# Performance work log

Hardware: AMD Instinct MI355X
Metric: run time of the kernel (lower is better)

The kernel has to match this reference:

```python
import jax, jax.numpy as jnp
import numpy as np

BLOCK = 64      # block_size
NRAND = 3       # num_random_blocks
NUM_HEAD = 16
HEAD_DIM = 64
HIDDEN = 1024
PEN = -10000.0  # HF attn_mask_penalty


def _sparse_attn(q, k, v, band_mask, from_mask, to_mask, blocked_mask, rand_attn):
    # q,k,v: [B,H,S,D]; BigBird block-sparse attention (HF math).
    B, H, S, D = q.shape
    b, r = BLOCK, NRAND
    n = S // b
    rsd = 1.0 / (D ** 0.5)

    bq = q.reshape(B, H, n, b, D)
    bk = k.reshape(B, H, n, b, D)
    bv = v.reshape(B, H, n, b, D)

    bi = jnp.arange(B)[:, None, None, None]
    hi = jnp.arange(H)[None, :, None, None]
    # gathered random key/value blocks: [B,H,n-2,r*b,D]
    gk = bk[bi, hi, rand_attn].reshape(B, H, n - 2, r * b, D)
    gv = bv[bi, hi, rand_attn].reshape(B, H, n - 2, r * b, D)
    # random-block mask: [B,H,n-2,b,r*b]
    rm = blocked_mask[bi, rand_attn].reshape(B, H, n - 2, r * b)
    rand_mask = jnp.einsum("blq,bhlk->bhlqk", blocked_mask[:, 1:-1], rm)

    ones = lambda shp: jnp.ones(shp, q.dtype)

    # ---- first query block: attends to everything ----
    p = jnp.einsum("bhqd,bhkd->bhqk", bq[:, :, 0], k) * rsd + (1.0 - to_mask) * PEN
    c0 = jnp.einsum("bhqk,bhkd->bhqd", jax.nn.softmax(p, -1), v)[:, :, None]

    # ---- second query block: blocks 0,1,2,last + random ----
    k1 = jnp.concatenate([bk[:, :, 0], bk[:, :, 1], bk[:, :, 2], bk[:, :, -1], gk[:, :, 0]], axis=2)
    v1 = jnp.concatenate([bv[:, :, 0], bv[:, :, 1], bv[:, :, 2], bv[:, :, -1], gv[:, :, 0]], axis=2)
    p = jnp.einsum("bhqd,bhkd->bhqk", bq[:, :, 1], k1) * rsd
    seq_pad = jnp.concatenate([to_mask[..., :3 * b], to_mask[..., -b:], ones((B, 1, 1, r * b))], axis=3)
    rand_pad = jnp.concatenate([ones((B, H, b, 4 * b)), rand_mask[:, :, 0]], axis=3)
    p = p + (1.0 - jnp.minimum(seq_pad, rand_pad)) * PEN
    c1 = jnp.einsum("bhqk,bhkd->bhqd", jax.nn.softmax(p, -1), v1)[:, :, None]

    # ---- middle blocks 2..n-3: band(3 blocks) + first + last + random ----
    ek = jnp.concatenate([bk[:, :, 1:-3], bk[:, :, 2:-2], bk[:, :, 3:-1]], axis=3)  # [B,H,n-4,3b,D]
    ev = jnp.concatenate([bv[:, :, 1:-3], bv[:, :, 2:-2], bv[:, :, 3:-1]], axis=3)
    mq = bq[:, :, 2:-2]                                                              # [B,H,n-4,b,D]
    inner = jnp.einsum("bhlqd,bhlkd->bhlqk", mq, ek) * rsd + (1.0 - band_mask) * PEN
    randp = jnp.einsum("bhlqd,bhlkd->bhlqk", mq, gk[:, :, 1:-1]) * rsd + (1.0 - rand_mask[:, :, 1:-1]) * PEN
    firstp = jnp.einsum("bhlqd,bhkd->bhlqk", mq, bk[:, :, 0]) * rsd + (1.0 - to_mask[..., :b][:, :, None]) * PEN
    lastp = jnp.einsum("bhlqd,bhkd->bhlqk", mq, bk[:, :, -1]) * rsd + (1.0 - to_mask[..., -b:][:, :, None]) * PEN
    band = jnp.concatenate([firstp, inner, randp, lastp], axis=-1)  # [B,H,n-4,b,(5+r)*b]
    a = jax.nn.softmax(band, -1)
    cm = jnp.einsum("bhlqk,bhlkd->bhlqd", a[..., b:4 * b], ev)
    cm = cm + jnp.einsum("bhlqk,bhlkd->bhlqd", a[..., 4 * b:-b], gv[:, :, 1:-1])
    cm = cm + jnp.einsum("bhlqk,bhkd->bhlqd", a[..., :b], bv[:, :, 0])
    cm = cm + jnp.einsum("bhlqk,bhkd->bhlqd", a[..., -b:], bv[:, :, -1])

    # ---- second-last query block: blocks 0,-3,-2,-1 + random ----
    k2 = jnp.concatenate([bk[:, :, 0], bk[:, :, -3], bk[:, :, -2], bk[:, :, -1], gk[:, :, -1]], axis=2)
    v2 = jnp.concatenate([bv[:, :, 0], bv[:, :, -3], bv[:, :, -2], bv[:, :, -1], gv[:, :, -1]], axis=2)
    p = jnp.einsum("bhqd,bhkd->bhqk", bq[:, :, -2], k2) * rsd
    seq_pad = jnp.concatenate([to_mask[..., :b], to_mask[..., -3 * b:], ones((B, 1, 1, r * b))], axis=3)
    rand_pad = jnp.concatenate([ones((B, H, b, 4 * b)), rand_mask[:, :, -1]], axis=3)
    p = p + (1.0 - jnp.minimum(seq_pad, rand_pad)) * PEN
    c2 = jnp.einsum("bhqk,bhkd->bhqd", jax.nn.softmax(p, -1), v2)[:, :, None]

    # ---- last query block: attends to everything ----
    p = jnp.einsum("bhqd,bhkd->bhqk", bq[:, :, -1], k) * rsd + (1.0 - to_mask) * PEN
    c3 = jnp.einsum("bhqk,bhkd->bhqd", jax.nn.softmax(p, -1), v)[:, :, None]

    ctx = jnp.concatenate([c0, c1, cm, c2, c3], axis=2).reshape(B, H, S, D)
    ctx = ctx * from_mask  # [B,1,S,1]
    return ctx.transpose(0, 2, 1, 3).reshape(B, S, H * D)


def setup_inputs() -> dict:
    key = jax.random.key(0)
    ks = jax.random.split(key, 12)
    B, L = 2, 4064
    S = 4096
    n = S // BLOCK
    sc = 0.02
    inp = {
        "X": jax.random.normal(ks[0], (B, L, HIDDEN), jnp.float32),
        "Wq": jax.random.normal(ks[1], (HIDDEN, NUM_HEAD * HEAD_DIM), jnp.float32) * sc,
        "b_q": jnp.zeros((NUM_HEAD * HEAD_DIM,), jnp.float32),
        "Wk": jax.random.normal(ks[2], (HIDDEN, NUM_HEAD * HEAD_DIM), jnp.float32) * sc,
        "b_k": jnp.zeros((NUM_HEAD * HEAD_DIM,), jnp.float32),
        "Wv": jax.random.normal(ks[3], (HIDDEN, NUM_HEAD * HEAD_DIM), jnp.float32) * sc,
        "b_v": jnp.zeros((NUM_HEAD * HEAD_DIM,), jnp.float32),
        "Wo": jax.random.normal(ks[4], (NUM_HEAD * HEAD_DIM, HIDDEN), jnp.float32) * sc,
        "b_o": jnp.zeros((HIDDEN,), jnp.float32),
        "band_mask": jnp.ones((B, 1, n - 4, BLOCK, 3 * BLOCK), jnp.float32),
        "from_mask": jnp.ones((B, 1, S, 1), jnp.float32),
        "to_mask": jnp.ones((B, 1, 1, S), jnp.float32),
        "blocked_encoder_mask": jnp.ones((B, n, BLOCK), jnp.float32),
        "rand_attn": jax.random.randint(ks[5], (B, NUM_HEAD, n - 2, NRAND), 0, n, jnp.int32),
    }
    return inp


def reference(X, Wq, b_q, Wk, b_k, Wv, b_v, Wo, b_o,
              band_mask, from_mask, to_mask, blocked_encoder_mask, rand_attn):
    B, L, _ = X.shape
    pad = BLOCK - L % BLOCK  # matches torch wrapper (pads full block if L % b == 0)
    Xp = jnp.pad(X, ((0, 0), (0, pad), (0, 0)))
    S = L + pad

    def proj(W, bias):
        return (Xp @ W + bias).reshape(B, S, NUM_HEAD, HEAD_DIM).transpose(0, 2, 1, 3)

    q, k, v = proj(Wq, b_q), proj(Wk, b_k), proj(Wv, b_v)
    attn = _sparse_attn(q, k, v, band_mask, from_mask, to_mask, blocked_encoder_mask, rand_attn)
    out = attn @ Wo + b_o
    return out[:, :L]
```

## Files before the change

### kernel.cpp

```cpp
#include <hip/hip_runtime.h>

#define BB 2
#define SEQ 4096
#define LQ 4064
#define HID 1024
#define NH 16
#define HD 64
#define NB 64
#define BLK 64
#define NR 3
#define PENV -10000.0f

typedef __bf16 bf16;
typedef __bf16 bf16x8 __attribute__((ext_vector_type(8)));
typedef float floatx4 __attribute__((ext_vector_type(4)));

#define MEMFENCE asm volatile("" ::: "memory")

__device__ inline floatx4 mfma16(bf16x8 a, bf16x8 b, floatx4 c) {
    return __builtin_amdgcn_mfma_f32_16x16x32_bf16(a, b, c, 0, 0, 0);
}

__device__ inline void async_ld16(const bf16* g, bf16* l) {
    __builtin_amdgcn_global_load_lds(
        (const __attribute__((address_space(1))) unsigned int*)g,
        (__attribute__((address_space(3))) unsigned int*)l, 16, 0, 0);
}

__device__ inline void stage_k2(const bf16* kkbh, bf16* dst, int kb0, int kb1, int tid) {
    #pragma unroll
    for (int it = 0; it < 2; it++) {
        int o = (it * 256 + tid) * 16;
        int row = o >> 7;
        int c16 = (o >> 4) & 7;
        int srcel = row * 64 + ((c16 ^ (row & 7)) << 3);
        async_ld16(kkbh + (size_t)kb0 * (BLK * HD) + srcel, dst + (o >> 1));
        async_ld16(kkbh + (size_t)kb1 * (BLK * HD) + srcel, dst + 4096 + (o >> 1));
    }
}

__global__ __launch_bounds__(256) void cast_pad_x(const float* __restrict__ X,
                                                  bf16* __restrict__ Xp) {
    int t = blockIdx.x * 256 + threadIdx.x;
    int c4 = t & 255;
    int row = t >> 8;
    int b = row >> 12;
    int s = row & 4095;
    float4 v = make_float4(0.f, 0.f, 0.f, 0.f);
    if (s < LQ) {
        v = reinterpret_cast<const float4*>(X + ((size_t)(b * LQ + s)) * HID)[c4];
    }
    union { bf16 h[4]; uint2 u; } o;
    o.h[0] = (bf16)v.x; o.h[1] = (bf16)v.y; o.h[2] = (bf16)v.z; o.h[3] = (bf16)v.w;
    *reinterpret_cast<uint2*>(Xp + (size_t)row * HID + c4 * 4) = o.u;
}

__global__ __launch_bounds__(256) void transpose_w(const float* __restrict__ Wq,
                                                   const float* __restrict__ Wk,
                                                   const float* __restrict__ Wv,
                                                   const float* __restrict__ Wo,
                                                   bf16* __restrict__ WqkvT,
                                                   bf16* __restrict__ WoT) {
    __shared__ float tile[64][65];
    int sel = blockIdx.z;
    const float* src = (sel == 0) ? Wq : (sel == 1) ? Wk : (sel == 2) ? Wv : Wo;
    bf16* dst = (sel < 3) ? (WqkvT + (size_t)sel * HID * HID) : WoT;
    int j0 = blockIdx.x * 64, k0 = blockIdx.y * 64;
    int tx = threadIdx.x, ty = threadIdx.y;
    for (int i = 0; i < 16; i++) {
        int k = ty + i * 4;
        tile[k][tx] = src[(size_t)(k0 + k) * HID + j0 + tx];
    }
    __syncthreads();
    for (int i = 0; i < 16; i++) {
        int j = ty + i * 4;
        dst[(size_t)(j0 + j) * HID + k0 + tx] = (bf16)tile[tx][j];
    }
}

__global__ __launch_bounds__(256) void transpose_band(const float* __restrict__ band,
                                                      float* __restrict__ bandT) {
    __shared__ float tile[64][65];
    int kt = blockIdx.x;
    int lrow = blockIdx.y;
    int b = blockIdx.z;
    const float* src = band + ((size_t)(b * (NB - 4) + lrow) * BLK) * 192;
    float* dst = bandT + ((size_t)(b * (NB - 4) + lrow) * 192) * BLK;
    int tx = threadIdx.x, ty = threadIdx.y;
    for (int i = 0; i < 16; i++) {
        int qq = i * 4 + ty;
        tile[qq][tx] = src[(size_t)qq * 192 + kt * 64 + tx];
    }
    __syncthreads();
    for (int i = 0; i < 16; i++) {
        int k = i * 4 + ty;
        dst[(size_t)(kt * 64 + k) * BLK + tx] = tile[tx][k];
    }
}

__global__ __launch_bounds__(256) void mask_viol(const float* __restrict__ tom,
                                                 const float* __restrict__ blocked,
                                                 const float* __restrict__ band,
                                                 int* __restrict__ flags) {
    int which = blockIdx.y, b = blockIdx.z;
    const float* src;
    size_t n;
    if (which == 0)      { src = tom     + (size_t)b * SEQ;                  n = SEQ; }
    else if (which == 1) { src = blocked + (size_t)b * NB * BLK;             n = NB * BLK; }
    else                 { src = band    + (size_t)b * (NB - 4) * BLK * 192; n = (size_t)(NB - 4) * BLK * 192; }
    const float4* s4 = (const float4*)src;
    size_t n4 = n >> 2;
    int bad = 0;
    for (size_t i = blockIdx.x * 256 + threadIdx.x; i < n4; i += 240 * 256) {
        float4 v = s4[i];
        bad |= (v.x != 1.0f) | (v.y != 1.0f) | (v.z != 1.0f) | (v.w != 1.0f);
    }
    if (__any(bad) && (threadIdx.x & 63) == 0)
        atomicOr(&flags[which * BB + b], 1);
}

__global__ __launch_bounds__(256) void gemm_qkv(const bf16* __restrict__ Xp,
                                                const bf16* __restrict__ WT,
                                                const float* __restrict__ bq,
                                                const float* __restrict__ bk,
                                                const float* __restrict__ bv,
                                                bf16* __restrict__ qo,
                                                bf16* __restrict__ ko,
                                                bf16* __restrict__ vt) {
    __shared__ __align__(16) char smem[36864];
    bf16* As = (bf16*)smem;
    bf16* Bs = As + 128 * 64;
    int tid = threadIdx.x;
    int wave = tid >> 6, lane = tid & 63;
    int quad = lane >> 4, lm = lane & 15;
    int id = blockIdx.x;
    int xcd = id & 7, slot = id >> 3;
    int tile_m = (xcd * 8 + (slot & 7)) * 128;
    int tile_n = (slot >> 3) * 128;
    int wm = (wave & 1) * 64, wn = (wave >> 1) * 64;

    floatx4 acc[4][4] = {};

    for (int k0 = 0; k0 < HID; k0 += 64) {
        __syncthreads();
        for (int it = 0; it < 4; it++) {
            int c = it * 256 + tid;
            int row = c >> 3, col = (c & 7) * 8;
            async_ld16(Xp + (size_t)(tile_m + row) * HID + k0 + col, &As[c * 8]);
            async_ld16(WT + (size_t)(tile_n + row) * HID + k0 + col, &Bs[c * 8]);
        }
        __syncthreads();
        for (int ks = 0; ks < 64; ks += 32) {
            bf16x8 a[4], b[4];
            for (int i = 0; i < 4; i++)
                a[i] = *reinterpret_cast<const bf16x8*>(&As[(wm + i * 16 + lm) * 64 + ks + quad * 8]);
            for (int j = 0; j < 4; j++)
                b[j] = *reinterpret_cast<const bf16x8*>(&Bs[(wn + j * 16 + lm) * 64 + ks + quad * 8]);
            for (int i = 0; i < 4; i++)
                for (int j = 0; j < 4; j++)
                    acc[i][j] = mfma16(a[i], b[j], acc[i][j]);
        }
    }

    int which = tile_n >> 10;
    int hc_base = (tile_n + wn) & 1023;
    int h = hc_base >> 6;
    const float* bias = (which == 0) ? bq : (which == 1) ? bk : bv;
    __syncthreads();
    bf16* ep = (bf16*)smem + wave * (64 * 72);

    if (which < 2) {
        #pragma unroll
        for (int i = 0; i < 4; i++)
            #pragma unroll
            for (int j = 0; j < 4; j++) {
                float bsv = bias[hc_base + j * 16 + lm];
                #pragma unroll
                for (int r = 0; r < 4; r++) {
                    float val = acc[i][j][r] + bsv;
                    if (which == 0) val *= 0.125f;
                    ep[(i * 16 + quad * 4 + r) * 72 + j * 16 + lm] = (bf16)val;
                }
            }
        __builtin_amdgcn_wave_barrier();
        int s_glob = tile_m + wm + lane;
        int b_ = s_glob >> 12, s = s_glob & 4095;
        bf16* dstb = ((which == 0) ? qo : ko) + ((size_t)((b_ * NH + h) * SEQ + s)) * HD;
        #pragma unroll
        for (int c = 0; c < 8; c++)
            *reinterpret_cast<uint4*>(dstb + c * 8) =
                *reinterpret_cast<const uint4*>(ep + lane * 72 + c * 8);
    } else {
        #pragma unroll
        for (int i = 0; i < 4; i++)
            #pragma unroll
            for (int j = 0; j < 4; j++) {
                float bsv = bias[hc_base + j * 16 + lm];
                #pragma unroll
                for (int r = 0; r < 4; r++) {
                    float val = acc[i][j][r] + bsv;
                    ep[(j * 16 + lm) * 72 + i * 16 + quad * 4 + r] = (bf16)val;
                }
            }
        __builtin_amdgcn_wave_barrier();
        int s_base = tile_m + wm;
        int b_ = s_base >> 12, s0 = s_base & 4095;
        bf16* dstb = vt + ((size_t)((b_ * NH + h) * HD + lane)) * SEQ + s0;
        #pragma unroll
        for (int c = 0; c < 8; c++)
            *reinterpret_cast<uint4*>(dstb + c * 8) =
                *reinterpret_cast<const uint4*>(ep + lane * 72 + c * 8);
    }
}

__global__ __launch_bounds__(256, 2) void attn_kernel(const bf16* __restrict__ q,
                                                      const bf16* __restrict__ kk,
                                                      const bf16* __restrict__ vt,
                                                      const float* __restrict__ bandT,
                                                      const float* __restrict__ fromm,
                                                      const float* __restrict__ tom,
                                                      const float* __restrict__ blocked,
                                                      const int* __restrict__ rand_attn,
                                                      const int* __restrict__ flags,
                                                      bf16* __restrict__ attn) {
    __shared__ __align__(16) char smem[32768];
    bf16* sK = (bf16*)smem;

    int tid = threadIdx.x, wave = tid >> 6, lane = tid & 63;
    int quad = lane >> 4, lm = lane & 15;
    int sw = lm & 7;
    int bh = blockIdx.x;
    int b = bh >> 4, h = bh & 15;
    size_t bh_base = (size_t)bh * SEQ * HD;
    int x = blockIdx.y;
    bool fullmode = (x < 8);
    int l, sub;
    if (fullmode) { l = (x >> 2) ? (NB - 1) : 0; sub = x & 3; }
    else          { l = x - 7;                   sub = wave;  }

    bool do_to = flags[b] != 0;
    bool do_bl = flags[BB + b] != 0;
    bool do_bd = flags[2 * BB + b] != 0;

    unsigned long long kbp = 0ull;
    unsigned int typ_p = 0u;
    if (!fullmode) {
        int base;
        if (l == 1) {
            kbp = (1ull << 8) | (2ull << 16) | ((unsigned long long)(NB - 1) << 24);
            base = 4;
        } else if (l == NB - 2) {
            kbp = ((unsigned long long)(NB - 3) << 8) | ((unsigned long long)(NB - 2) << 16) |
                  ((unsigned long long)(NB - 1) << 24);
            base = 4;
        } else {
            kbp = ((unsigned long long)(l - 1) << 8) | ((unsigned long long)l << 16) |
                  ((unsigned long long)(l + 1) << 24) | ((unsigned long long)(NB - 1) << 32);
            typ_p = (1u << 4) | (2u << 8) | (3u << 12);
            base = 5;
        }
        const int* ra = rand_attn + ((size_t)(b * NH + h) * (NB - 2) + (l - 1)) * NR;
        #pragma unroll
        for (int r = 0; r < NR; r++) {
            int rv = __builtin_amdgcn_readfirstlane(ra[r]);
            kbp   |= (unsigned long long)(rv & 63) << ((base + r) * 8);
            typ_p |= 4u << ((base + r) * 4);
        }
        for (int i = base + NR; i < 8; i++) typ_p |= 5u << (i * 4);
    }

    bf16x8 aq0 = *reinterpret_cast<const bf16x8*>(
        q + bh_base + (size_t)(l * BLK + sub * 16 + lm) * HD + quad * 8);
    bf16x8 aq1 = *reinterpret_cast<const bf16x8*>(
        q + bh_base + (size_t)(l * BLK + sub * 16 + lm) * HD + 32 + quad * 8);
    float mq = blocked[((size_t)b * NB + l) * BLK + sub * 16 + lm];

    if (!fullmode) {
        MEMFENCE;
        int a0 = (int)((kbp >> 0) & 63),  a1 = (int)((kbp >> 8) & 63);
        int b0 = (int)((kbp >> 16) & 63), b1 = (int)((kbp >> 24) & 63);
        stage_k2(kk + bh_base, sK + 0,    a0, a1, tid);
        stage_k2(kk + bh_base, sK + 8192, b0, b1, tid);
        MEMFENCE;
    }

    floatx4 ctx[4] = {};
    float mrun = -1e30f, lrun = 0.f;

    int sbase = ((quad & 1) << 5) + lm;
    int fhi = quad >> 1;

    int nch = fullmode ? 8 : 4;
    for (int ch = 0; ch < nch; ch++) {
        int i0 = ch * 2, i1 = i0 + 1;
        int kb0, kb1, ty0, ty1;
        if (fullmode) {
            kb0 = __builtin_amdgcn_readfirstlane(wave * 16 + i0);
            kb1 = kb0 + 1;
            ty0 = 0; ty1 = 0;
        } else {
            kb0 = __builtin_amdgcn_readfirstlane((int)((kbp >> (i0 * 8)) & 63));
            kb1 = __builtin_amdgcn_readfirstlane((int)((kbp >> (i1 * 8)) & 63));
            ty0 = (int)((typ_p >> (i0 * 4)) & 15);
            ty1 = (int)((typ_p >> (i1 * 4)) & 15);
        }

        const bf16* v0p = vt + bh_base + (size_t)kb0 * BLK;
        bf16x8 vf0[4][2];
        #pragma unroll
        for (int dj = 0; dj < 4; dj++) {
            vf0[dj][0] = *reinterpret_cast<const bf16x8*>(v0p + (size_t)(dj * 16 + lm) * SEQ + quad * 8);
            vf0[dj][1] = *reinterpret_cast<const bf16x8*>(v0p + (size_t)(dj * 16 + lm) * SEQ + 32 + quad * 8);
        }
        MEMFENCE;

        floatx4 sc[2][4];
        if (!fullmode) {
            if (ch < 3) asm volatile("s_waitcnt vmcnt(8)" ::: "memory");
            else        asm volatile("s_waitcnt vmcnt(16)" ::: "memory");
            __builtin_amdgcn_s_barrier();
            const bf16* kbuf = sK + (ch & 1) * 8192;
            #pragma unroll
            for (int u = 0; u < 2; u++) {
                bf16x8 ka[4], kb_[4];
                #pragma unroll
                for (int f = 0; f < 4; f++) {
                    int rowb = (f * 16 + lm) * 64;
                    ka[f]  = *reinterpret_cast<const bf16x8*>(
                        kbuf + u * 4096 + rowb + ((quad ^ sw) << 3));
                    kb_[f] = *reinterpret_cast<const bf16x8*>(
                        kbuf + u * 4096 + rowb + (((quad | 4) ^ sw) << 3));
                }
                #pragma unroll
                for (int f = 0; f < 4; f++) {
                    floatx4 z = {0.f, 0.f, 0.f, 0.f};
                    z = mfma16(ka[f], aq0, z);
                    z = mfma16(kb_[f], aq1, z);
                    sc[u][f] = z;
                }
            }
        } else {
            const bf16* k0p = kk + bh_base + (size_t)kb0 * (BLK * HD);
            const bf16* k1p = kk + bh_base + (size_t)kb1 * (BLK * HD);
            bf16x8 kfa[2][4], kfb[2][4];
            #pragma unroll
            for (int f = 0; f < 4; f++) {
                kfa[0][f] = *reinterpret_cast<const bf16x8*>(k0p + (f * 16 + lm) * HD + quad * 8);
                kfb[0][f] = *reinterpret_cast<const bf16x8*>(k0p + (f * 16 + lm) * HD + 32 + quad * 8);
                kfa[1][f] = *reinterpret_cast<const bf16x8*>(k1p + (f * 16 + lm) * HD + quad * 8);
                kfb[1][f] = *reinterpret_cast<const bf16x8*>(k1p + (f * 16 + lm) * HD + 32 + quad * 8);
            }
            #pragma unroll
            for (int u = 0; u < 2; u++)
                #pragma unroll
                for (int f = 0; f < 4; f++) {
                    floatx4 z = {0.f, 0.f, 0.f, 0.f};
                    z = mfma16(kfa[u][f], aq0, z);
                    z = mfma16(kfb[u][f], aq1, z);
                    sc[u][f] = z;
                }
        }

        const bf16* v1p = vt + bh_base + (size_t)kb1 * BLK;
        bf16x8 vf1[4][2];
        #pragma unroll
        for (int dj = 0; dj < 4; dj++) {
            vf1[dj][0] = *reinterpret_cast<const bf16x8*>(v1p + (size_t)(dj * 16 + lm) * SEQ + quad * 8);
            vf1[dj][1] = *reinterpret_cast<const bf16x8*>(v1p + (size_t)(dj * 16 + lm) * SEQ + 32 + quad * 8);
        }
        MEMFENCE;

        {
            int kbs[2] = {kb0, kb1};
            int tys[2] = {ty0, ty1};
            #pragma unroll
            for (int u = 0; u < 2; u++) {
                int kb = kbs[u], typ = tys[u];
                if (typ == 0) {
                    if (do_to) {
                        #pragma unroll
                        for (int f = 0; f < 4; f++) {
                            float4 t4 = *reinterpret_cast<const float4*>(
                                tom + (size_t)b * SEQ + kb * BLK + f * 16 + quad * 4);
                            sc[u][f][0] += (1.f - t4.x) * PENV;
                            sc[u][f][1] += (1.f - t4.y) * PENV;
                            sc[u][f][2] += (1.f - t4.z) * PENV;
                            sc[u][f][3] += (1.f - t4.w) * PENV;
                        }
                    }
                } else if (typ == 4) {
                    if (do_bl) {
                        #pragma unroll
                        for (int f = 0; f < 4; f++) {
                            float4 t4 = *reinterpret_cast<const float4*>(
                                blocked + ((size_t)b * NB + kb) * BLK + f * 16 + quad * 4);
                            sc[u][f][0] += (1.f - mq * t4.x) * PENV;
                            sc[u][f][1] += (1.f - mq * t4.y) * PENV;
                            sc[u][f][2] += (1.f - mq * t4.z) * PENV;
                            sc[u][f][3] += (1.f - mq * t4.w) * PENV;
                        }
                    }
                } else if (typ != 5) {
                    if (do_bd) {
                        int t = typ - 1;
                        const float* bp = bandT + ((size_t)(b * (NB - 4) + (l - 2)) * 192 + t * 64) * BLK;
                        #pragma unroll
                        for (int f = 0; f < 4; f++)
                            #pragma unroll
                            for (int r = 0; r < 4; r++) {
                                float bm = bp[(size_t)(f * 16 + quad * 4 + r) * BLK + sub * 16 + lm];
                                sc[u][f][r] += (1.f - bm) * PENV;
                            }
                    }
                } else {
                    #pragma unroll
                    for (int f = 0; f < 4; f++)
                        #pragma unroll
                        for (int r = 0; r < 4; r++) sc[u][f][r] += PENV;
                }
            }
        }

        float mx = -1e30f;
        #pragma unroll
        for (int u = 0; u < 2; u++)
            #pragma unroll
            for (int f = 0; f < 4; f++)
                #pragma unroll
                for (int r = 0; r < 4; r++) mx = fmaxf(mx, sc[u][f][r]);
        float a16 = __shfl_xor(mx, 16, 64);
        float a32 = __shfl_xor(mx, 32, 64);
        float a48 = __shfl_xor(mx, 48, 64);
        mx = fmaxf(fmaxf(mx, a16), fmaxf(a32, a48));
        float mnew = fmaxf(mrun, mx);
        float scale = __expf(mrun - mnew);
        #pragma unroll
        for (int dj = 0; dj < 4; dj++) ctx[dj] *= scale;
        mrun = mnew;

        float rs = 0.f;
        uint2 pk[2][4];
        #pragma unroll
        for (int u = 0; u < 2; u++)
            #pragma unroll
            for (int f = 0; f < 4; f++) {
                float p0 = __expf(sc[u][f][0] - mnew);
                float p1 = __expf(sc[u][f][1] - mnew);
                float p2 = __expf(sc[u][f][2] - mnew);
                float p3 = __expf(sc[u][f][3] - mnew);
                rs += (p0 + p1) + (p2 + p3);
                union { bf16 hh[4]; uint2 u2; } pu;
                pu.hh[0] = (bf16)p0; pu.hh[1] = (bf16)p1;
                pu.hh[2] = (bf16)p2; pu.hh[3] = (bf16)p3;
                pk[u][f] = pu.u2;
            }
        lrun = lrun * scale + rs;

        bf16x8 pb[2][2];
        #pragma unroll
        for (int u = 0; u < 2; u++) {
            unsigned g0x[4], g0y[4], g1x[4], g1y[4];
            #pragma unroll
            for (int f = 0; f < 4; f++) {
                g0x[f] = (unsigned)__shfl((int)pk[u][f].x, sbase, 64);
                g0y[f] = (unsigned)__shfl((int)pk[u][f].y, sbase, 64);
                g1x[f] = (unsigned)__shfl((int)pk[u][f].x, sbase + 16, 64);
                g1y[f] = (unsigned)__shfl((int)pk[u][f].y, sbase + 16, 64);
            }
            union { unsigned v[4]; bf16x8 hv; } lo, hi;
            lo.v[0] = fhi ? g0x[1] : g0x[0];
            lo.v[1] = fhi ? g0y[1] : g0y[0];
            lo.v[2] = fhi ? g1x[1] : g1x[0];
            lo.v[3] = fhi ? g1y[1] : g1y[0];
            hi.v[0] = fhi ? g0x[3] : g0x[2];
            hi.v[1] = fhi ? g0y[3] : g0y[2];
            hi.v[2] = fhi ? g1x[3] : g1x[2];
            hi.v[3] = fhi ? g1y[3] : g1y[2];
            pb[u][0] = lo.hv;
            pb[u][1] = hi.hv;
        }

        if (!fullmode && ch >= 1 && ch + 1 < 4) {
            int na = __builtin_amdgcn_readfirstlane((int)((kbp >> ((ch + 1) * 16)) & 63));
            int nb = __builtin_amdgcn_readfirstlane((int)((kbp >> ((ch + 1) * 16 + 8)) & 63));
            stage_k2(kk + bh_base, sK + ((ch + 1) & 1) * 8192, na, nb, tid);
            MEMFENCE;
        }

        #pragma unroll
        for (int dj = 0; dj < 4; dj++) {
            ctx[dj] = mfma16(vf0[dj][0], pb[0][0], ctx[dj]);
            ctx[dj] = mfma16(vf0[dj][1], pb[0][1], ctx[dj]);
        }
        #pragma unroll
        for (int dj = 0; dj < 4; dj++) {
            ctx[dj] = mfma16(vf1[dj][0], pb[1][0], ctx[dj]);
            ctx[dj] = mfma16(vf1[dj][1], pb[1][1], ctx[dj]);
        }
    }

    {
        float b16 = __shfl_xor(lrun, 16, 64);
        float b32 = __shfl_xor(lrun, 32, 64);
        float b48 = __shfl_xor(lrun, 48, 64);
        lrun = (lrun + b16) + (b32 + b48);
    }

    if (!fullmode) {
        int sq = l * BLK + sub * 16 + lm;
        float w = (1.f / lrun) * fromm[(size_t)b * SEQ + sq];
        bf16* dst = attn + ((size_t)(b * SEQ + sq)) * HID + h * HD;
        #pragma unroll
        for (int dj = 0; dj < 4; dj++) {
            union { bf16 hh[4]; uint2 u2; } o;
            #pragma unroll
            for (int r = 0; r < 4; r++) o.hh[r] = (bf16)(ctx[dj][r] * w);
            *reinterpret_cast<uint2*>(dst + dj * 16 + quad * 4) = o.u2;
        }
    } else {
        float* ctxL = (float*)smem;
        float* mL   = (float*)(smem + 16384);
        float* lL   = (float*)(smem + 16640);
        __syncthreads();
        #pragma unroll
        for (int dj = 0; dj < 4; dj++)
            #pragma unroll
            for (int r = 0; r < 4; r++)
                ctxL[wave * 1024 + (dj * 16 + quad * 4 + r) * 16 + lm] = ctx[dj][r];
        if (quad == 0) { mL[wave * 16 + lm] = mrun; lL[wave * 16 + lm] = lrun; }
        __syncthreads();
        int qq = tid & 15, dbase = (tid >> 4) * 4;
        float M = -1e30f;
        for (int w = 0; w < 4; w++) M = fmaxf(M, mL[w * 16 + qq]);
        float e[4], Lt = 0.f;
        for (int w = 0; w < 4; w++) { e[w] = __expf(mL[w * 16 + qq] - M); Lt += lL[w * 16 + qq] * e[w]; }
        int sq = l * BLK + sub * 16 + qq;
        float wgt = (1.f / Lt) * fromm[(size_t)b * SEQ + sq];
        union { bf16 hh[4]; uint2 u2; } o;
        #pragma unroll
        for (int dd = 0; dd < 4; dd++) {
            float acc = 0.f;
            for (int w = 0; w < 4; w++) acc += ctxL[w * 1024 + (dbase + dd) * 16 + qq] * e[w];
            o.hh[dd] = (bf16)(acc * wgt);
        }
        *reinterpret_cast<uint2*>(attn + ((size_t)(b * SEQ + sq)) * HID + h * HD + dbase) = o.u2;
    }
}

__global__ __launch_bounds__(256) void gemm_out(const bf16* __restrict__ A,
                                                const bf16* __restrict__ WoT,
                                                const float* __restrict__ bo,
                                                float* __restrict__ out) {
    __shared__ __align__(16) bf16 As[128 * 64];
    __shared__ __align__(16) bf16 Bs[128 * 64];
    int tid = threadIdx.x;
    int wave = tid >> 6, lane = tid & 63;
    int quad = lane >> 4, lm = lane & 15;
    int id = blockIdx.x;
    int xcd = id & 7, slot = id >> 3;
    int tile_m = (xcd * 8 + (slot & 7)) * 128;
    int tile_n = (slot >> 3) * 128;
    int wm = (wave & 1) * 64, wn = (wave >> 1) * 64;

    floatx4 acc[4][4] = {};

    for (int k0 = 0; k0 < HID; k0 += 64) {
        __syncthreads();
        for (int it = 0; it < 4; it++) {
            int c = it * 256 + tid;
            int row = c >> 3, col = (c & 7) * 8;
            async_ld16(A + (size_t)(tile_m + row) * HID + k0 + col, &As[c * 8]);
            async_ld16(WoT + (size_t)(tile_n + row) * HID + k0 + col, &Bs[c * 8]);
        }
        __syncthreads();
        for (int ks = 0; ks < 64; ks += 32) {
            bf16x8 a[4], b[4];
            for (int i = 0; i < 4; i++)
                a[i] = *reinterpret_cast<const bf16x8*>(&As[(wm + i * 16 + lm) * 64 + ks + quad * 8]);
            for (int j = 0; j < 4; j++)
                b[j] = *reinterpret_cast<const bf16x8*>(&Bs[(wn + j * 16 + lm) * 64 + ks + quad * 8]);
            for (int i = 0; i < 4; i++)
                for (int j = 0; j < 4; j++)
                    acc[i][j] = mfma16(a[i], b[j], acc[i][j]);
        }
    }

    for (int i = 0; i < 4; i++) {
        for (int j = 0; j < 4; j++) {
            int nn = tile_n + wn + j * 16 + lm;
            float bsv = bo[nn];
            for (int r = 0; r < 4; r++) {
                int mm = tile_m + wm + i * 16 + quad * 4 + r;
                int b_ = mm >> 12, s = mm & 4095;
                if (s < LQ)
                    out[((size_t)(b_ * LQ + s)) * HID + nn] = acc[i][j][r] + bsv;
            }
        }
    }
}

extern "C" void kernel_launch(void* const* d_in, const int* in_sizes, int n_in,
                              void* d_out, int out_size, void* d_ws, size_t ws_size,
                              hipStream_t stream) {
    const float* X       = (const float*)d_in[0];
    const float* Wq      = (const float*)d_in[1];
    const float* bq      = (const float*)d_in[2];
    const float* Wk      = (const float*)d_in[3];
    const float* bk      = (const float*)d_in[4];
    const float* Wv      = (const float*)d_in[5];
    const float* bv      = (const float*)d_in[6];
    const float* Wo      = (const float*)d_in[7];
    const float* bo      = (const float*)d_in[8];
    const float* band    = (const float*)d_in[9];
    const float* fromm   = (const float*)d_in[10];
    const float* tom     = (const float*)d_in[11];
    const float* blocked = (const float*)d_in[12];
    const int*   randa   = (const int*)d_in[13];
    float* out = (float*)d_out;

    char* ws = (char*)d_ws;
    bf16* Xp    = (bf16*)(ws + 0);
    bf16* WqkvT = (bf16*)(ws + 16777216);
    bf16* WoT   = (bf16*)(ws + 23068672);
    bf16* qb    = (bf16*)(ws + 25165824);
    bf16* kb    = (bf16*)(ws + 41943040);
    bf16* vtb   = (bf16*)(ws + 58720256);
    bf16* attnb = Xp;
    float* bandT = (float*)WqkvT;
    int* flagsp = (int*)(ws + 16777216 + 5898240);

    cast_pad_x<<<dim3(8192), dim3(256), 0, stream>>>(X, Xp);
    transpose_w<<<dim3(16, 16, 4), dim3(64, 4), 0, stream>>>(Wq, Wk, Wv, Wo, WqkvT, WoT);
    gemm_qkv<<<dim3(1536), dim3(256), 0, stream>>>(Xp, WqkvT, bq, bk, bv, qb, kb, vtb);
    transpose_band<<<dim3(3, NB - 4, BB), dim3(64, 4), 0, stream>>>(band, bandT);
    hipMemsetAsync(flagsp, 0, 3 * BB * sizeof(int), stream);
    mask_viol<<<dim3(240, 3, BB), dim3(256), 0, stream>>>(tom, blocked, band, flagsp);
    attn_kernel<<<dim3(BB * NH, 70), dim3(256), 0, stream>>>(qb, kb, vtb, bandT, fromm, tom,
                                                             blocked, randa, flagsp, attnb);
    gemm_out<<<dim3(512), dim3(256), 0, stream>>>(attnb, WoT, bo, out);
}
```

Before: 341.7 us.

## Double-buffer output GEMM LDS tiles and raise wave priority around MFMA blocks

The output projection GEMM now uses two LDS buffers, so the async global-to-LDS load for the next K tile is issued while MFMAs run on the current one. This removes one barrier per iteration and hides load latency. In the attention kernel, s_setprio brackets the QK and PV MFMA sections so waves doing matrix work get scheduling priority. The GEMM doubles its LDS use to 64KB, which may lower occupancy. The next tile's loads are issued without an explicit wait before the tile is consumed, so correctness depends on the barrier draining outstanding loads.

```diff
diff --git a/kernel.cpp b/kernel.cpp
--- a/kernel.cpp
+++ b/kernel.cpp
@@ -320,6 +320,7 @@
             else        asm volatile("s_waitcnt vmcnt(16)" ::: "memory");
             __builtin_amdgcn_s_barrier();
             const bf16* kbuf = sK + (ch & 1) * 8192;
+            __builtin_amdgcn_s_setprio(1);
             #pragma unroll
             for (int u = 0; u < 2; u++) {
                 bf16x8 ka[4], kb_[4];
@@ -339,6 +340,7 @@
                     sc[u][f] = z;
                 }
             }
+            __builtin_amdgcn_s_setprio(0);
         } else {
             const bf16* k0p = kk + bh_base + (size_t)kb0 * (BLK * HD);
             const bf16* k1p = kk + bh_base + (size_t)kb1 * (BLK * HD);
@@ -350,6 +352,7 @@
                 kfa[1][f] = *reinterpret_cast<const bf16x8*>(k1p + (f * 16 + lm) * HD + quad * 8);
                 kfb[1][f] = *reinterpret_cast<const bf16x8*>(k1p + (f * 16 + lm) * HD + 32 + quad * 8);
             }
+            __builtin_amdgcn_s_setprio(1);
             #pragma unroll
             for (int u = 0; u < 2; u++)
                 #pragma unroll
@@ -359,6 +362,7 @@
                     z = mfma16(kfb[u][f], aq1, z);
                     sc[u][f] = z;
                 }
+            __builtin_amdgcn_s_setprio(0);
         }
 
         const bf16* v1p = vt + bh_base + (size_t)kb1 * BLK;
@@ -487,6 +491,7 @@
             MEMFENCE;
         }
 
+        __builtin_amdgcn_s_setprio(1);
         #pragma unroll
         for (int dj = 0; dj < 4; dj++) {
             ctx[dj] = mfma16(vf0[dj][0], pb[0][0], ctx[dj]);
@@ -497,6 +502,7 @@
             ctx[dj] = mfma16(vf1[dj][0], pb[1][0], ctx[dj]);
             ctx[dj] = mfma16(vf1[dj][1], pb[1][1], ctx[dj]);
         }
+        __builtin_amdgcn_s_setprio(0);
     }
 
     {
@@ -551,8 +557,7 @@
                                                 const bf16* __restrict__ WoT,
                                                 const float* __restrict__ bo,
                                                 float* __restrict__ out) {
-    __shared__ __align__(16) bf16 As[128 * 64];
-    __shared__ __align__(16) bf16 Bs[128 * 64];
+    __shared__ __align__(16) char smem[65536];
     int tid = threadIdx.x;
     int wave = tid >> 6, lane = tid & 63;
     int quad = lane >> 4, lm = lane & 15;
@@ -564,15 +569,33 @@
 
     floatx4 acc[4][4] = {};
 
-    for (int k0 = 0; k0 < HID; k0 += 64) {
-        __syncthreads();
+    {
+        bf16* base = (bf16*)smem;
+        #pragma unroll
         for (int it = 0; it < 4; it++) {
             int c = it * 256 + tid;
             int row = c >> 3, col = (c & 7) * 8;
-            async_ld16(A + (size_t)(tile_m + row) * HID + k0 + col, &As[c * 8]);
-            async_ld16(WoT + (size_t)(tile_n + row) * HID + k0 + col, &Bs[c * 8]);
-        }
-        __syncthreads();
+            async_ld16(A + (size_t)(tile_m + row) * HID + col, &base[c * 8]);
+            async_ld16(WoT + (size_t)(tile_n + row) * HID + col, &base[8192 + c * 8]);
+        }
+    }
+    __syncthreads();
+
+    for (int t = 0; t < 16; t++) {
+        if (t < 15) {
+            bf16* base = (bf16*)smem + ((t + 1) & 1) * 16384;
+            int k0 = (t + 1) * 64;
+            #pragma unroll
+            for (int it = 0; it < 4; it++) {
+                int c = it * 256 + tid;
+                int row = c >> 3, col = (c & 7) * 8;
+                async_ld16(A + (size_t)(tile_m + row) * HID + k0 + col, &base[c * 8]);
+                async_ld16(WoT + (size_t)(tile_n + row) * HID + k0 + col, &base[8192 + c * 8]);
+            }
+        }
+        const bf16* As = (const bf16*)smem + (t & 1) * 16384;
+        const bf16* Bs = As + 8192;
+        #pragma unroll
         for (int ks = 0; ks < 64; ks += 32) {
             bf16x8 a[4], b[4];
             for (int i = 0; i < 4; i++)
@@ -583,6 +606,7 @@
                 for (int j = 0; j < 4; j++)
                     acc[i][j] = mfma16(a[i], b[j], acc[i][j]);
         }
+        __syncthreads();
     }
 
     for (int i = 0; i < 4; i++) {
```

After: 334.1 us. -2.2%, faster.
